# Performance work log

Hardware: AMD Instinct MI355X
Metric: run time of the kernel (lower is better)

Reference implementation:

```python
import jax, jax.numpy as jnp
import numpy as np

K = 7            # filter_size
N_ITERS = 5
SXY_G = 3.0      # gaussian spatial sigma
SRGB = 10.0      # bilateral color sigma
COMPAT_G = 3.0
COMPAT_B = 10.0


def _gaussian_kernel(size, sigma):
    coords = jnp.arange(size, dtype=jnp.float32) - (size - 1) / 2.0
    g = jnp.exp(-coords ** 2 / (2.0 * sigma ** 2))
    g = g / g.sum()
    return g[None, :] * g[:, None]  # (K, K), row-major flatten matches torch view


def _unfold(x, k):
    # x: (B,C,H,W) -> (B,C,k*k,H,W), zero padding, patch elements in row-major
    # order (ki*k + kj), matching F.unfold + view(B,C,k*k,H,W).
    B, C, H, W = x.shape
    p = k // 2
    xp = jnp.pad(x, ((0, 0), (0, 0), (p, p), (p, p)))
    patches = [xp[:, :, i:i + H, j:j + W] for i in range(k) for j in range(k)]
    return jnp.stack(patches, axis=2)


def setup_inputs() -> dict:
    key = jax.random.key(0)
    k1, k2 = jax.random.split(key)
    B, C, H, W = 2, 29, 256, 256
    unary = jax.random.normal(k1, (B, C, H, W), dtype=jnp.float32)
    img = jax.random.uniform(k2, (B, 3, H, W), dtype=jnp.float32) * 255.0  # RGB [0,255]
    return {"unary": unary, "img": img}


def reference(unary, img):
    # unary: (B,C,H,W) logits (neg log prob); img: (B,3,H,W)
    spatial = _gaussian_kernel(K, SXY_G).reshape(-1)        # (K*K,)
    sw = spatial[None, None, :, None, None]                 # (1,1,K2,1,1)

    # Precompute bilateral weights once (as in the torch module)
    img_unfold = _unfold(img, K)                            # (B,3,K2,H,W)
    diff_sq = ((img_unfold - img[:, :, None]) ** 2).sum(axis=1, keepdims=True)
    bilateral = jnp.exp(-diff_sq / (2.0 * SRGB ** 2)) * sw  # (B,1,K2,H,W)

    q = jax.nn.softmax(-unary, axis=1)
    for _ in range(N_ITERS):
        q_unf = _unfold(q, K)                   # (B,C,K2,H,W)
        msg_b = (q_unf * bilateral).sum(axis=2) # bilateral message
        # depthwise gaussian conv with zero padding == gaussian-weighted patch sum
        msg_g = (q_unf * sw).sum(axis=2)
        pairwise = COMPAT_G * msg_g + COMPAT_B * msg_b
        q = jax.nn.softmax(-unary + pairwise, axis=1)
    return q
```

## Files before the change

### kernel.cpp

```cpp
#include <hip/hip_runtime.h>
#include <hip/hip_fp16.h>

#define CNUM 29
#define HH 256
#define WW 256
#define BB 2
#define KK 7
#define HALO 3
#define TX 32
#define TY 4
#define LW (TX + 2*HALO)
#define LH (TY + 2*HALO)
#define NPIX (LH*LW)
#define HWP (HH*WW)

__device__ constexpr float GW[KK] = {
    0.106287146f, 0.140321912f, 0.165770643f, 0.175240699f,
    0.165770643f, 0.140321912f, 0.106287146f};

__device__ __forceinline__ unsigned packh2(float a, float b) {
    __half2 h = __floats2half2_rn(a, b);
    return *reinterpret_cast<unsigned*>(&h);
}
__device__ __forceinline__ float2 unpkh2(unsigned u) {
    __half2 h = *reinterpret_cast<__half2*>(&u);
    return __half22float2(h);
}

template <bool FIRST, bool LAST>
__global__ __launch_bounds__(256) void crf_iter(const float* __restrict__ unary,
                                                const float* __restrict__ img,
                                                const uint4* __restrict__ qin,
                                                uint4* __restrict__ qout,
                                                uint4* __restrict__ uh,
                                                float* __restrict__ outf) {
    __shared__ uint4  s_q4[NPIX * 4];
    __shared__ float2 s_im2[NPIX];
    __shared__ float  s_imz[NPIX];

    const int tid = threadIdx.x;
    const bool isA = tid < 128;
    const int lid = tid & 127;
    const int tx = lid & (TX - 1);
    const int ty = lid >> 5;

    const int flat = (blockIdx.z << 9) | (blockIdx.y << 3) | blockIdx.x;
    const int sid  = ((flat & 7) << 7) | (flat >> 3);
    const int b    = sid >> 9;
    const int rem  = sid & 511;
    const int by   = (rem >> 3) * TY;
    const int bx   = (rem & 7) * TX;
    const int pix  = (by + ty) * WW + (bx + tx);

    const float* ubase = unary + (size_t)b * CNUM * HWP;
    const float* imgb  = img + (size_t)b * 3 * HWP;

    if (FIRST) {
        for (int t = tid; t < NPIX; t += 256) {
            int r = t / LW, cc = t - r * LW;
            int gy = by + r - HALO, gx = bx + cc - HALO;
            bool ok = (gy >= 0) & (gy < HH) & (gx >= 0) & (gx < WW);
            int goff = ok ? gy * WW + gx : 0;
            float i0 = imgb[goff], i1 = imgb[HWP + goff], i2 = imgb[2 * HWP + goff];
            if (!ok) { i0 = 0.f; i1 = 0.f; i2 = 0.f; }
            float2 v2; v2.x = i0; v2.y = i1;
            s_im2[t] = v2; s_imz[t] = i2;

            float nu[CNUM];
            float mm = -1e30f;
#pragma unroll
            for (int c = 0; c < CNUM; ++c) {
                nu[c] = -ubase[(size_t)c * HWP + goff];
                mm = fmaxf(mm, nu[c]);
            }
            bool interior = (r >= HALO) & (r < LH - HALO) & (cc >= HALO) & (cc < LW - HALO);
            if (interior) {
                uint4* up = uh + ((size_t)b * HWP + goff) * 4;
                uint4 u0, u1, u2, u3;
                u0.x = packh2(nu[0],  nu[1]);  u0.y = packh2(nu[2],  nu[3]);
                u0.z = packh2(nu[4],  nu[5]);  u0.w = packh2(nu[6],  nu[7]);
                u1.x = packh2(nu[8],  nu[9]);  u1.y = packh2(nu[10], nu[11]);
                u1.z = packh2(nu[12], nu[13]); u1.w = packh2(nu[14], nu[15]);
                u2.x = packh2(nu[16], nu[17]); u2.y = packh2(nu[18], nu[19]);
                u2.z = packh2(nu[20], nu[21]); u2.w = packh2(nu[22], nu[23]);
                u3.x = packh2(nu[24], nu[25]); u3.y = packh2(nu[26], nu[27]);
                u3.z = packh2(nu[28], 0.f);    u3.w = 0u;
                up[0] = u0; up[1] = u1; up[2] = u2; up[3] = u3;
            }
            float ss = 0.f;
            float v[CNUM];
#pragma unroll
            for (int c = 0; c < CNUM; ++c) { v[c] = __expf(nu[c] - mm); ss += v[c]; }
            float inv = ok ? 1.f / ss : 0.f;
#pragma unroll
            for (int c = 0; c < CNUM; ++c) v[c] *= inv;
            const int swz = (t >> 1) & 3;
            uint4 p0, p1, p2, p3;
            p0.x = packh2(v[0],  v[1]);  p0.y = packh2(v[2],  v[3]);
            p0.z = packh2(v[4],  v[5]);  p0.w = packh2(v[6],  v[7]);
            p1.x = packh2(v[8],  v[9]);  p1.y = packh2(v[10], v[11]);
            p1.z = packh2(v[12], v[13]); p1.w = packh2(v[14], v[15]);
            p2.x = packh2(v[16], v[17]); p2.y = packh2(v[18], v[19]);
            p2.z = packh2(v[20], v[21]); p2.w = packh2(v[22], v[23]);
            p3.x = packh2(v[24], v[25]); p3.y = packh2(v[26], v[27]);
            p3.z = packh2(v[28], 0.f);   p3.w = 0u;
            s_q4[t * 4 + (0 ^ swz)] = p0;
            s_q4[t * 4 + (1 ^ swz)] = p1;
            s_q4[t * 4 + (2 ^ swz)] = p2;
            s_q4[t * 4 + (3 ^ swz)] = p3;
        }
    } else {
        int t = tid;
        int r = t / LW, cc = t - r * LW;
        int gy = by + r - HALO, gx = bx + cc - HALO;
        bool ok = (gy >= 0) & (gy < HH) & (gx >= 0) & (gx < WW);
        int goff = ok ? gy * WW + gx : 0;
        float i0 = imgb[goff], i1 = imgb[HWP + goff], i2 = imgb[2 * HWP + goff];
        const uint4* qp = qin + ((size_t)b * HWP + goff) * 4;
        uint4 p0 = qp[0], p1 = qp[1], p2 = qp[2], p3 = qp[3];

        int t2 = tid + 256;
        bool has2 = t2 < NPIX;
        int r2 = t2 / LW, cc2 = t2 - r2 * LW;
        int gy2 = by + r2 - HALO, gx2 = bx + cc2 - HALO;
        bool ok2 = has2 & (gy2 >= 0) & (gy2 < HH) & (gx2 >= 0) & (gx2 < WW);
        int goff2 = ok2 ? gy2 * WW + gx2 : 0;
        float j0 = 0.f, j1 = 0.f, j2 = 0.f;
        uint4 s0, s1, s2, s3;
        if (has2) {
            j0 = imgb[goff2]; j1 = imgb[HWP + goff2]; j2 = imgb[2 * HWP + goff2];
            const uint4* qp2 = qin + ((size_t)b * HWP + goff2) * 4;
            s0 = qp2[0]; s1 = qp2[1]; s2 = qp2[2]; s3 = qp2[3];
        }
        if (!ok) {
            i0 = 0.f; i1 = 0.f; i2 = 0.f;
            p0.x = p0.y = p0.z = p0.w = 0u; p1.x = p1.y = p1.z = p1.w = 0u;
            p2.x = p2.y = p2.z = p2.w = 0u; p3.x = p3.y = p3.z = p3.w = 0u;
        }
        float2 v2; v2.x = i0; v2.y = i1;
        s_im2[t] = v2; s_imz[t] = i2;
        const int swz = (t >> 1) & 3;
        s_q4[t * 4 + (0 ^ swz)] = p0;
        s_q4[t * 4 + (1 ^ swz)] = p1;
        s_q4[t * 4 + (2 ^ swz)] = p2;
        s_q4[t * 4 + (3 ^ swz)] = p3;
        if (has2) {
            if (!ok2) {
                j0 = 0.f; j1 = 0.f; j2 = 0.f;
                s0.x = s0.y = s0.z = s0.w = 0u; s1.x = s1.y = s1.z = s1.w = 0u;
                s2.x = s2.y = s2.z = s2.w = 0u; s3.x = s3.y = s3.z = s3.w = 0u;
            }
            float2 w2; w2.x = j0; w2.y = j1;
            s_im2[t2] = w2; s_imz[t2] = j2;
            const int swz2 = (t2 >> 1) & 3;
            s_q4[t2 * 4 + (0 ^ swz2)] = s0;
            s_q4[t2 * 4 + (1 ^ swz2)] = s1;
            s_q4[t2 * 4 + (2 ^ swz2)] = s2;
            s_q4[t2 * 4 + (3 ^ swz2)] = s3;
        }
    }
    __syncthreads();

    const int tc = (ty + HALO) * LW + (tx + HALO);
    const float2 cv = s_im2[tc];
    const float c0 = cv.x;
    const float c1 = cv.y;
    const float c2 = s_imz[tc];

    float acc[CNUM];
#pragma unroll
    for (int c = 0; c < CNUM; ++c) acc[c] = 0.f;

#define TAP_BODY(ii)                                                        \
    {                                                                       \
        const int t = (ty + (ii)) * LW + (tx + j);                          \
        float2 iv = s_im2[t];                                               \
        float d0 = iv.x - c0;                                               \
        float d1 = iv.y - c1;                                               \
        float d2 = s_imz[t] - c2;                                           \
        float dsq = d0 * d0 + d1 * d1 + d2 * d2;                            \
        float w = (GW[(ii)] * GW[j]) * (3.0f + 10.0f * __expf(dsq * -0.005f)); \
        const int t4 = t * 4;                                               \
        const int swz = (t >> 1) & 3;                                       \
        uint4 q0 = s_q4[t4 + (0 ^ swz)];                                    \
        uint4 q1 = s_q4[t4 + (1 ^ swz)];                                    \
        uint4 q2 = s_q4[t4 + (2 ^ swz)];                                    \
        uint4 q3 = s_q4[t4 + (3 ^ swz)];                                    \
        const unsigned* u0 = &q0.x;                                         \
        const unsigned* u1 = &q1.x;                                         \
        const unsigned* u2 = &q2.x;                                         \
        _Pragma("unroll")                                                   \
        for (int k = 0; k < 4; ++k) {                                       \
            float2 f = unpkh2(u0[k]);                                       \
            acc[2 * k]     += w * f.x;                                      \
            acc[2 * k + 1] += w * f.y;                                      \
        }                                                                   \
        _Pragma("unroll")                                                   \
        for (int k = 0; k < 4; ++k) {                                       \
            float2 f = unpkh2(u1[k]);                                       \
            acc[8 + 2 * k]     += w * f.x;                                  \
            acc[8 + 2 * k + 1] += w * f.y;                                  \
        }                                                                   \
        _Pragma("unroll")                                                   \
        for (int k = 0; k < 4; ++k) {                                       \
            float2 f = unpkh2(u2[k]);                                       \
            acc[16 + 2 * k]     += w * f.x;                                 \
            acc[16 + 2 * k + 1] += w * f.y;                                 \
        }                                                                   \
        {                                                                   \
            float2 f = unpkh2(q3.x);                                        \
            acc[24] += w * f.x; acc[25] += w * f.y;                         \
            f = unpkh2(q3.y);                                               \
            acc[26] += w * f.x; acc[27] += w * f.y;                         \
            f = unpkh2(q3.z);                                               \
            acc[28] += w * f.x;                                             \
        }                                                                   \
    }

    if (isA) {
#pragma unroll
        for (int i = 4; i < KK; ++i)
#pragma unroll
            for (int j = 0; j < KK; ++j) TAP_BODY(i)
    } else {
#pragma unroll
        for (int i = 0; i < 4; ++i)
#pragma unroll
            for (int j = 0; j < KK; ++j) TAP_BODY(i)
    }
#undef TAP_BODY

    __syncthreads();
    float* s_part = reinterpret_cast<float*>(s_q4);
    if (!isA) {
#pragma unroll
        for (int c = 0; c < CNUM; ++c) s_part[c * 128 + lid] = acc[c];
    }
    __syncthreads();

    if (isA) {
        float l[CNUM];
        if (FIRST) {
#pragma unroll
            for (int c = 0; c < CNUM; ++c)
                l[c] = acc[c] + s_part[c * 128 + lid] - ubase[(size_t)c * HWP + pix];
        } else {
            const uint4* up = uh + ((size_t)b * HWP + pix) * 4;
            uint4 n0 = up[0], n1 = up[1], n2 = up[2], n3 = up[3];
            const unsigned* w0 = &n0.x;
            const unsigned* w1 = &n1.x;
            const unsigned* w2 = &n2.x;
            float nu[CNUM];
#pragma unroll
            for (int k = 0; k < 4; ++k) {
                float2 f = unpkh2(w0[k]); nu[2 * k] = f.x; nu[2 * k + 1] = f.y;
            }
#pragma unroll
            for (int k = 0; k < 4; ++k) {
                float2 f = unpkh2(w1[k]); nu[8 + 2 * k] = f.x; nu[8 + 2 * k + 1] = f.y;
            }
#pragma unroll
            for (int k = 0; k < 4; ++k) {
                float2 f = unpkh2(w2[k]); nu[16 + 2 * k] = f.x; nu[16 + 2 * k + 1] = f.y;
            }
            { float2 f = unpkh2(n3.x); nu[24] = f.x; nu[25] = f.y; }
            { float2 f = unpkh2(n3.y); nu[26] = f.x; nu[27] = f.y; }
            { float2 f = unpkh2(n3.z); nu[28] = f.x; }
#pragma unroll
            for (int c = 0; c < CNUM; ++c)
                l[c] = acc[c] + s_part[c * 128 + lid] + nu[c];
        }
        float m = l[0];
#pragma unroll
        for (int c = 1; c < CNUM; ++c) m = fmaxf(m, l[c]);
        float ss = 0.f;
#pragma unroll
        for (int c = 0; c < CNUM; ++c) { l[c] = __expf(l[c] - m); ss += l[c]; }
        float inv = 1.0f / ss;

        if (LAST) {
            float* qo = outf + (size_t)b * CNUM * HWP + pix;
#pragma unroll
            for (int c = 0; c < CNUM; ++c) qo[(size_t)c * HWP] = l[c] * inv;
        } else {
            uint4 p0, p1, p2, p3;
            p0.x = packh2(l[0] * inv,  l[1] * inv);
            p0.y = packh2(l[2] * inv,  l[3] * inv);
            p0.z = packh2(l[4] * inv,  l[5] * inv);
            p0.w = packh2(l[6] * inv,  l[7] * inv);
            p1.x = packh2(l[8] * inv,  l[9] * inv);
            p1.y = packh2(l[10] * inv, l[11] * inv);
            p1.z = packh2(l[12] * inv, l[13] * inv);
            p1.w = packh2(l[14] * inv, l[15] * inv);
            p2.x = packh2(l[16] * inv, l[17] * inv);
            p2.y = packh2(l[18] * inv, l[19] * inv);
            p2.z = packh2(l[20] * inv, l[21] * inv);
            p2.w = packh2(l[22] * inv, l[23] * inv);
            p3.x = packh2(l[24] * inv, l[25] * inv);
            p3.y = packh2(l[26] * inv, l[27] * inv);
            p3.z = packh2(l[28] * inv, 0.f);
            p3.w = 0u;
            uint4* qo = qout + ((size_t)b * HWP + pix) * 4;
            qo[0] = p0; qo[1] = p1; qo[2] = p2; qo[3] = p3;
        }
    }
}

extern "C" void kernel_launch(void* const* d_in, const int* in_sizes, int n_in,
                              void* d_out, int out_size, void* d_ws, size_t ws_size,
                              hipStream_t stream) {
    const float* unary = (const float*)d_in[0];
    const float* img   = (const float*)d_in[1];
    const size_t QBYTES = (size_t)BB * HWP * 64;
    uint4* qA = (uint4*)d_ws;
    uint4* qB = (uint4*)((char*)d_ws + QBYTES);
    uint4* uh = (uint4*)((char*)d_ws + 2 * QBYTES);
    float* outf = (float*)d_out;

    dim3 grid(WW / TX, HH / TY, BB);
    crf_iter<true,  false><<<grid, 256, 0, stream>>>(unary, img, qB, qA, uh, outf);
    crf_iter<false, false><<<grid, 256, 0, stream>>>(unary, img, qA, qB, uh, outf);
    crf_iter<false, false><<<grid, 256, 0, stream>>>(unary, img, qB, qA, uh, outf);
    crf_iter<false, false><<<grid, 256, 0, stream>>>(unary, img, qA, qB, uh, outf);
    crf_iter<false, true ><<<grid, 256, 0, stream>>>(unary, img, qB, qA, uh, outf);
}
```

Measured before the change: 93.70 us.

## Split softmax epilogue across both thread halves and drop max subtraction

Previously only the first 128 threads ran the final softmax and store. Now each half handles part of the channels (16 and 13). Partial exp sums are combined through a small shared reduction, and the upper half-precision words of q are passed through shared memory so the first half can issue the packed store. The softmax max-subtraction is removed in both the initial and per-iteration softmax, which trades numerical safety for large logits against fewer instructions. s_setprio is also raised around the tap loop. An extra barrier is added in the non-last path.

```diff
diff --git a/kernel.cpp b/kernel.cpp
--- a/kernel.cpp
+++ b/kernel.cpp
@@ -37,6 +37,7 @@
     __shared__ uint4  s_q4[NPIX * 4];
     __shared__ float2 s_im2[NPIX];
     __shared__ float  s_imz[NPIX];
+    __shared__ float  s_red[2][128];
 
     const int tid = threadIdx.x;
     const bool isA = tid < 128;
@@ -67,12 +68,8 @@
             s_im2[t] = v2; s_imz[t] = i2;
 
             float nu[CNUM];
-            float mm = -1e30f;
-#pragma unroll
-            for (int c = 0; c < CNUM; ++c) {
-                nu[c] = -ubase[(size_t)c * HWP + goff];
-                mm = fmaxf(mm, nu[c]);
-            }
+#pragma unroll
+            for (int c = 0; c < CNUM; ++c) nu[c] = -ubase[(size_t)c * HWP + goff];
             bool interior = (r >= HALO) & (r < LH - HALO) & (cc >= HALO) & (cc < LW - HALO);
             if (interior) {
                 uint4* up = uh + ((size_t)b * HWP + goff) * 4;
@@ -90,7 +87,7 @@
             float ss = 0.f;
             float v[CNUM];
 #pragma unroll
-            for (int c = 0; c < CNUM; ++c) { v[c] = __expf(nu[c] - mm); ss += v[c]; }
+            for (int c = 0; c < CNUM; ++c) { v[c] = __expf(nu[c]); ss += v[c]; }
             float inv = ok ? 1.f / ss : 0.f;
 #pragma unroll
             for (int c = 0; c < CNUM; ++c) v[c] *= inv;
@@ -217,6 +214,7 @@
         }                                                                   \
     }
 
+    __builtin_amdgcn_s_setprio(1);
     if (isA) {
 #pragma unroll
         for (int i = 4; i < KK; ++i)
@@ -228,29 +226,32 @@
 #pragma unroll
             for (int j = 0; j < KK; ++j) TAP_BODY(i)
     }
+    __builtin_amdgcn_s_setprio(0);
 #undef TAP_BODY
 
     __syncthreads();
     float* s_part = reinterpret_cast<float*>(s_q4);
-    if (!isA) {
-#pragma unroll
-        for (int c = 0; c < CNUM; ++c) s_part[c * 128 + lid] = acc[c];
+    if (isA) {
+#pragma unroll
+        for (int c = 16; c < CNUM; ++c) s_part[c * 128 + lid] = acc[c];
+    } else {
+#pragma unroll
+        for (int c = 0; c < 16; ++c) s_part[c * 128 + lid] = acc[c];
     }
     __syncthreads();
 
+    float l[16];
+    float ss_loc = 0.f;
     if (isA) {
-        float l[CNUM];
+        float nu[16];
         if (FIRST) {
 #pragma unroll
-            for (int c = 0; c < CNUM; ++c)
-                l[c] = acc[c] + s_part[c * 128 + lid] - ubase[(size_t)c * HWP + pix];
+            for (int c = 0; c < 16; ++c) nu[c] = -ubase[(size_t)c * HWP + pix];
         } else {
             const uint4* up = uh + ((size_t)b * HWP + pix) * 4;
-            uint4 n0 = up[0], n1 = up[1], n2 = up[2], n3 = up[3];
+            uint4 n0 = up[0], n1 = up[1];
             const unsigned* w0 = &n0.x;
             const unsigned* w1 = &n1.x;
-            const unsigned* w2 = &n2.x;
-            float nu[CNUM];
 #pragma unroll
             for (int k = 0; k < 4; ++k) {
                 float2 f = unpkh2(w0[k]); nu[2 * k] = f.x; nu[2 * k + 1] = f.y;
@@ -259,31 +260,66 @@
             for (int k = 0; k < 4; ++k) {
                 float2 f = unpkh2(w1[k]); nu[8 + 2 * k] = f.x; nu[8 + 2 * k + 1] = f.y;
             }
+        }
+#pragma unroll
+        for (int c = 0; c < 16; ++c) {
+            l[c] = __expf(acc[c] + s_part[c * 128 + lid] + nu[c]);
+            ss_loc += l[c];
+        }
+    } else {
+        float nu[13];
+        if (FIRST) {
+#pragma unroll
+            for (int c = 0; c < 13; ++c) nu[c] = -ubase[(size_t)(16 + c) * HWP + pix];
+        } else {
+            const uint4* up = uh + ((size_t)b * HWP + pix) * 4;
+            uint4 n2 = up[2], n3 = up[3];
+            const unsigned* w2 = &n2.x;
 #pragma unroll
             for (int k = 0; k < 4; ++k) {
-                float2 f = unpkh2(w2[k]); nu[16 + 2 * k] = f.x; nu[16 + 2 * k + 1] = f.y;
-            }
-            { float2 f = unpkh2(n3.x); nu[24] = f.x; nu[25] = f.y; }
-            { float2 f = unpkh2(n3.y); nu[26] = f.x; nu[27] = f.y; }
-            { float2 f = unpkh2(n3.z); nu[28] = f.x; }
-#pragma unroll
-            for (int c = 0; c < CNUM; ++c)
-                l[c] = acc[c] + s_part[c * 128 + lid] + nu[c];
-        }
-        float m = l[0];
-#pragma unroll
-        for (int c = 1; c < CNUM; ++c) m = fmaxf(m, l[c]);
-        float ss = 0.f;
-#pragma unroll
-        for (int c = 0; c < CNUM; ++c) { l[c] = __expf(l[c] - m); ss += l[c]; }
-        float inv = 1.0f / ss;
-
-        if (LAST) {
-            float* qo = outf + (size_t)b * CNUM * HWP + pix;
-#pragma unroll
-            for (int c = 0; c < CNUM; ++c) qo[(size_t)c * HWP] = l[c] * inv;
+                float2 f = unpkh2(w2[k]); nu[2 * k] = f.x; nu[2 * k + 1] = f.y;
+            }
+            { float2 f = unpkh2(n3.x); nu[8]  = f.x; nu[9]  = f.y; }
+            { float2 f = unpkh2(n3.y); nu[10] = f.x; nu[11] = f.y; }
+            { float2 f = unpkh2(n3.z); nu[12] = f.x; }
+        }
+#pragma unroll
+        for (int c = 0; c < 13; ++c) {
+            l[c] = __expf(acc[16 + c] + s_part[(16 + c) * 128 + lid] + nu[c]);
+            ss_loc += l[c];
+        }
+    }
+    s_red[isA ? 0 : 1][lid] = ss_loc;
+    __syncthreads();
+    const float inv = 1.0f / (s_red[0][lid] + s_red[1][lid]);
+
+    if (LAST) {
+        float* qo = outf + (size_t)b * CNUM * HWP + pix;
+        if (isA) {
+#pragma unroll
+            for (int c = 0; c < 16; ++c) qo[(size_t)c * HWP] = l[c] * inv;
         } else {
-            uint4 p0, p1, p2, p3;
+#pragma unroll
+            for (int c = 0; c < 13; ++c) qo[(size_t)(16 + c) * HWP] = l[c] * inv;
+        }
+    } else {
+        uint4* s_xf = reinterpret_cast<uint4*>(s_q4);
+        if (!isA) {
+            uint4 p2, p3;
+            p2.x = packh2(l[0] * inv,  l[1] * inv);
+            p2.y = packh2(l[2] * inv,  l[3] * inv);
+            p2.z = packh2(l[4] * inv,  l[5] * inv);
+            p2.w = packh2(l[6] * inv,  l[7] * inv);
+            p3.x = packh2(l[8] * inv,  l[9] * inv);
+            p3.y = packh2(l[10] * inv, l[11] * inv);
+            p3.z = packh2(l[12] * inv, 0.f);
+            p3.w = 0u;
+            s_xf[lid * 2 + 0] = p2;
+            s_xf[lid * 2 + 1] = p3;
+        }
+        __syncthreads();
+        if (isA) {
+            uint4 p0, p1;
             p0.x = packh2(l[0] * inv,  l[1] * inv);
             p0.y = packh2(l[2] * inv,  l[3] * inv);
             p0.z = packh2(l[4] * inv,  l[5] * inv);
@@ -292,14 +328,8 @@
             p1.y = packh2(l[10] * inv, l[11] * inv);
             p1.z = packh2(l[12] * inv, l[13] * inv);
             p1.w = packh2(l[14] * inv, l[15] * inv);
-            p2.x = packh2(l[16] * inv, l[17] * inv);
-            p2.y = packh2(l[18] * inv, l[19] * inv);
-            p2.z = packh2(l[20] * inv, l[21] * inv);
-            p2.w = packh2(l[22] * inv, l[23] * inv);
-            p3.x = packh2(l[24] * inv, l[25] * inv);
-            p3.y = packh2(l[26] * inv, l[27] * inv);
-            p3.z = packh2(l[28] * inv, 0.f);
-            p3.w = 0u;
+            uint4 p2 = s_xf[lid * 2 + 0];
+            uint4 p3 = s_xf[lid * 2 + 1];
             uint4* qo = qout + ((size_t)b * HWP + pix) * 4;
             qo[0] = p0; qo[1] = p1; qo[2] = p2; qo[3] = p3;
         }
```

New measurement: 90.14 us (median of 2 runs). 1.04x faster.
